# Optimization experiments

Measured on AMD Instinct MI355X. Metric: run time of the kernel, lower is better.

Reference implementation:

```python
import jax
import jax.numpy as jnp
import numpy as np
from jax import lax

GAMMA = 0.99  # cfg.offline_gamma
TAU = 0.95    # cfg.tau (GAE lambda)
T = 4_194_304  # trajectory length (many episodes concatenated, separated by mask=0)


def setup_inputs() -> dict:
    key = jax.random.key(0)
    k1, k2, k3, k4 = jax.random.split(key, 4)
    rewards = jax.random.normal(k1, (T, 1), dtype=jnp.float32)
    values = jax.random.normal(k2, (T, 1), dtype=jnp.float32)        # critic.get_max_value(states)
    next_values = jax.random.normal(k3, (T, 1), dtype=jnp.float32)   # critic.get_max_value(next_states) (bootstrap=True)
    masks = jax.random.randint(k4, (T, 1), 0, 2).astype(jnp.int32)   # 1 = non-terminal, 0 = episode end
    return {"rewards": rewards, "values": values, "next_values": next_values, "masks": masks}


def reference(rewards, values, next_values, masks):
    """Faithful translation of A2C.get_phi's reversed loop as a single lax.scan.

    returns[i]    = r[i] + gamma * (prev_return * m[i] + (1 - m[i]) * next_values[i])
    deltas[i]     = r[i] + gamma * prev_value * m[i] - values[i]
    advantages[i] = deltas[i] + gamma * tau * prev_advantage * m[i]
    with prev_* taken from step i+1 (zeros past the end).
    """
    m = masks.astype(rewards.dtype)  # [T,1]

    def step(carry, xs):
        prev_ret, prev_val, prev_adv = carry  # each [1]
        r, v, nv, mm = xs                     # each [1]
        ret = r + GAMMA * (prev_ret * mm + (1.0 - mm) * nv)
        delta = r + GAMMA * prev_val * mm - v
        adv = delta + GAMMA * TAU * prev_adv * mm
        return (ret, v, adv), (adv, ret)

    zero = jnp.zeros((1,), dtype=rewards.dtype)
    init = (zero, zero, zero)
    _, (advantages, returns) = lax.scan(
        step, init, (rewards, values, next_values, m), reverse=True
    )
    return advantages, returns  # each [T,1]
```

## Files before the change

kernel.cpp:

```cpp
#include <hip/hip_runtime.h>

#define GAMMA 0.99f
#define TAU   0.95f
#define GTAU  (GAMMA * TAU)

constexpr int SEQ   = 16;
constexpr int BLK   = 256;
constexpr int CHUNK = BLK * SEQ;

__device__ __forceinline__ void post_compose(float& A, float& B, float rA, float rB) {
    B = fmaf(A, rB, B);
    A *= rA;
}
__device__ __forceinline__ void pre_compose(float& A, float& B, float lA, float lB) {
    B = fmaf(lA, B, lB);
    A *= lA;
}

__global__ __launch_bounds__(BLK, 4) void k_fused1(
    const float* __restrict__ r, const float* __restrict__ v,
    const float* __restrict__ nv, const int* __restrict__ m,
    float* __restrict__ out_adv, float* __restrict__ out_ret, int T)
{
    const int  tid  = threadIdx.x;
    const int  lane = tid & 63;
    const int  w    = tid >> 6;
    const int  c    = (int)blockIdx.x;
    const long base = (long)c * CHUNK + (long)tid * SEQ;
    const long p    = (long)(c + 1) * CHUNK;

    __shared__ float wSum[4][4];
    __shared__ float s_cb[2];

    float pm = 0.f, pr = 0.f, pv = 0.f, pv1 = 0.f, pnv = 0.f;
    if (w == 0 && p < (long)T) {
        long i = p + lane;
        if (i < (long)T) {
            pm  = (float)m[i];
            pr  = r[i];
            pv  = v[i];
            pv1 = (i + 1 < (long)T) ? v[i + 1] : 0.f;
            pnv = nv[i];
        }
    }

    float delta[SEQ], dd[SEQ];
    unsigned vbits = 0, mbits = 0;
    float Aa = 1.f, Ba = 0.f, Ar = 1.f, Br = 0.f;
    const bool full = (base + SEQ <= (long)T);

    if (full) {
        vbits = 0xFFFFu;
        float rr[SEQ], vv[SEQ + 1], nn[SEQ], fmv[SEQ];
        #pragma unroll
        for (int q = 0; q < SEQ / 4; ++q) {
            float4 t0 = ((const float4*)(r  + base))[q];
            rr[4*q+0]=t0.x; rr[4*q+1]=t0.y; rr[4*q+2]=t0.z; rr[4*q+3]=t0.w;
            float4 t1 = ((const float4*)(v  + base))[q];
            vv[4*q+0]=t1.x; vv[4*q+1]=t1.y; vv[4*q+2]=t1.z; vv[4*q+3]=t1.w;
            float4 t2 = ((const float4*)(nv + base))[q];
            nn[4*q+0]=t2.x; nn[4*q+1]=t2.y; nn[4*q+2]=t2.z; nn[4*q+3]=t2.w;
            int4   t3 = ((const int4*)(m   + base))[q];
            fmv[4*q+0]=(float)t3.x; fmv[4*q+1]=(float)t3.y;
            fmv[4*q+2]=(float)t3.z; fmv[4*q+3]=(float)t3.w;
        }
        vv[SEQ] = (base + SEQ < (long)T) ? v[base + SEQ] : 0.f;
        #pragma unroll
        for (int i = SEQ - 1; i >= 0; --i) {
            if (fmv[i] != 0.f) mbits |= (1u << i);
            delta[i] = rr[i] + GAMMA * fmv[i] * vv[i+1] - vv[i];
            dd[i]    = rr[i] + GAMMA * (1.f - fmv[i]) * nn[i];
            pre_compose(Aa, Ba, GTAU * fmv[i], delta[i]);
            pre_compose(Ar, Br, GAMMA * fmv[i], dd[i]);
        }
    } else {
        #pragma unroll
        for (int ii = 0; ii < SEQ; ++ii) {
            int i = SEQ - 1 - ii;
            long idx = base + i;
            bool val = idx < (long)T;
            float rr  = val ? r[idx]  : 0.f;
            float vv0 = val ? v[idx]  : 0.f;
            float vv1 = (idx + 1 < (long)T) ? v[idx + 1] : 0.f;
            float nn  = val ? nv[idx] : 0.f;
            float fmv = val ? (float)m[idx] : 0.f;
            if (val) vbits |= (1u << i);
            if (val && fmv != 0.f) mbits |= (1u << i);
            delta[i] = val ? (rr + GAMMA * fmv * vv1 - vv0) : 0.f;
            dd[i]    = val ? (rr + GAMMA * (1.f - fmv) * nn) : 0.f;
            pre_compose(Aa, Ba, val ? GTAU * fmv : 1.f, delta[i]);
            pre_compose(Ar, Br, val ? GAMMA * fmv : 1.f, dd[i]);
        }
    }

    #pragma unroll
    for (int st = 1; st < 64; st <<= 1) {
        float oAa = __shfl_down(Aa, st);
        float oBa = __shfl_down(Ba, st);
        float oAr = __shfl_down(Ar, st);
        float oBr = __shfl_down(Br, st);
        if (lane + st < 64) {
            post_compose(Aa, Ba, oAa, oBa);
            post_compose(Ar, Br, oAr, oBr);
        }
    }
    float eAa = __shfl_down(Aa, 1);
    float eBa = __shfl_down(Ba, 1);
    float eAr = __shfl_down(Ar, 1);
    float eBr = __shfl_down(Br, 1);
    if (lane == 63) { eAa=1.f; eBa=0.f; eAr=1.f; eBr=0.f; }

    if (lane == 0) { wSum[w][0]=Aa; wSum[w][1]=Ba; wSum[w][2]=Ar; wSum[w][3]=Br; }
    __syncthreads();

    float WAa=1.f, WBa=0.f, WAr=1.f, WBr=0.f;
    for (int j = 3; j > w; --j) {
        pre_compose(WAa, WBa, wSum[j][0], wSum[j][1]);
        pre_compose(WAr, WBr, wSum[j][2], wSum[j][3]);
    }

    if (w == 0) {
        float MAa=1.f, MBa=0.f, MAr=1.f, MBr=0.f;
        if (p < (long)T) {
            {
                long i = p + lane;
                bool have = i < (long)T;
                float aA=1.f, aB=0.f, rA_=1.f, rB_=0.f;
                if (have) {
                    aA  = GTAU * pm;
                    aB  = pr + GAMMA * pm * pv1 - pv;
                    rA_ = GAMMA * pm;
                    rB_ = pr + GAMMA * (1.f - pm) * pnv;
                }
                bool term = (!have) || (pm == 0.f);
                unsigned long long bz = __ballot(term);
                #pragma unroll
                for (int st = 1; st < 64; st <<= 1) {
                    float oAa = __shfl_down(aA,  st);
                    float oBa = __shfl_down(aB,  st);
                    float oAr = __shfl_down(rA_, st);
                    float oBr = __shfl_down(rB_, st);
                    if (lane + st < 64) {
                        post_compose(aA,  aB,  oAa, oBa);
                        post_compose(rA_, rB_, oAr, oBr);
                    }
                }
                MAa = __shfl(aA, 0);  MBa = __shfl(aB, 0);
                MAr = __shfl(rA_, 0); MBr = __shfl(rB_, 0);
                if (bz != 0ull) goto carry_done;
            }
            for (long jb = p + 64; ; jb += 64) {
                long i = jb + lane;
                bool have = i < (long)T;
                float aA=1.f, aB=0.f, rA_=1.f, rB_=0.f;
                float mi = 0.f;
                if (have) {
                    mi = (float)m[i];
                    float ri  = r[i];
                    float vi  = v[i];
                    float vi1 = (i + 1 < (long)T) ? v[i + 1] : 0.f;
                    float nvi = nv[i];
                    aA  = GTAU * mi;
                    aB  = ri + GAMMA * mi * vi1 - vi;
                    rA_ = GAMMA * mi;
                    rB_ = ri + GAMMA * (1.f - mi) * nvi;
                }
                bool term = (!have) || (mi == 0.f);
                unsigned long long bz = __ballot(term);
                #pragma unroll
                for (int st = 1; st < 64; st <<= 1) {
                    float oAa = __shfl_down(aA,  st);
                    float oBa = __shfl_down(aB,  st);
                    float oAr = __shfl_down(rA_, st);
                    float oBr = __shfl_down(rB_, st);
                    if (lane + st < 64) {
                        post_compose(aA,  aB,  oAa, oBa);
                        post_compose(rA_, rB_, oAr, oBr);
                    }
                }
                float bAa = __shfl(aA, 0),  bBa = __shfl(aB, 0);
                float bAr = __shfl(rA_, 0), bBr = __shfl(rB_, 0);
                post_compose(MAa, MBa, bAa, bBa);
                post_compose(MAr, MBr, bAr, bBr);
                if (bz != 0ull) break;
            }
        }
carry_done:
        if (lane == 0) {
            s_cb[0] = MBa;
            s_cb[1] = MBr;
        }
    }
    __syncthreads();
    const float cbA = s_cb[0];
    const float cbR = s_cb[1];

    float xa = fmaf(WAa, cbA, WBa);
    float xr = fmaf(WAr, cbR, WBr);
    xa = fmaf(eAa, xa, eBa);
    xr = fmaf(eAr, xr, eBr);

    if (full) {
        #pragma unroll
        for (int q = SEQ / 4 - 1; q >= 0; --q) {
            float ta[4], tr[4];
            #pragma unroll
            for (int k = 3; k >= 0; --k) {
                int i = 4 * q + k;
                float a  = (mbits >> i & 1u) ? GTAU  : 0.f;
                float cc = (mbits >> i & 1u) ? GAMMA : 0.f;
                xa = fmaf(a,  xa, delta[i]);
                xr = fmaf(cc, xr, dd[i]);
                ta[k] = xa; tr[k] = xr;
            }
            ((float4*)(out_adv + base))[q] = make_float4(ta[0], ta[1], ta[2], ta[3]);
            ((float4*)(out_ret + base))[q] = make_float4(tr[0], tr[1], tr[2], tr[3]);
        }
    } else {
        #pragma unroll
        for (int i = SEQ - 1; i >= 0; --i) {
            bool val = (vbits >> i) & 1u;
            float a  = val ? ((mbits >> i & 1u) ? GTAU  : 0.f) : 1.f;
            float cc = val ? ((mbits >> i & 1u) ? GAMMA : 0.f) : 1.f;
            xa = fmaf(a,  xa, delta[i]);
            xr = fmaf(cc, xr, dd[i]);
            if (base + i < (long)T) {
                out_adv[base + i] = xa;
                out_ret[base + i] = xr;
            }
        }
    }
}

extern "C" void kernel_launch(void* const* d_in, const int* in_sizes, int n_in,
                              void* d_out, int out_size, void* d_ws, size_t ws_size,
                              hipStream_t stream) {
    const float* r  = (const float*)d_in[0];
    const float* v  = (const float*)d_in[1];
    const float* nv = (const float*)d_in[2];
    const int*   m  = (const int*)d_in[3];
    const int T = in_sizes[0];
    const int nblk = (T + CHUNK - 1) / CHUNK;

    float* out_adv = (float*)d_out;
    float* out_ret = (float*)d_out + T;

    k_fused1<<<nblk, BLK, 0, stream>>>(r, v, nv, m, out_adv, out_ret, T);
}
```

Measured before the change: 26.17 us.

## Shrink per-thread sequence to 4 and share next value via wave shuffle

Reduces elements per thread from 16 to 4, so each thread does a single float4 load per input and the grid has four times as many blocks. The value at the following position is taken from the neighbouring lane with a shuffle rather than reloaded, and full-tile detection moves to wave granularity. The launch-bounds occupancy hint is removed. More blocks means more work in the decoupled carry-propagation chain and more scan overhead per element, traded for lower register pressure and more memory parallelism.

```diff
diff --git a/kernel.cpp b/kernel.cpp
--- a/kernel.cpp
+++ b/kernel.cpp
@@ -4,7 +4,7 @@
 #define TAU   0.95f
 #define GTAU  (GAMMA * TAU)
 
-constexpr int SEQ   = 16;
+constexpr int SEQ   = 4;
 constexpr int BLK   = 256;
 constexpr int CHUNK = BLK * SEQ;
 
@@ -17,7 +17,7 @@
     A *= lA;
 }
 
-__global__ __launch_bounds__(BLK, 4) void k_fused1(
+__global__ __launch_bounds__(BLK) void k_fused1(
     const float* __restrict__ r, const float* __restrict__ v,
     const float* __restrict__ nv, const int* __restrict__ m,
     float* __restrict__ out_adv, float* __restrict__ out_ret, int T)
@@ -47,30 +47,28 @@
     float delta[SEQ], dd[SEQ];
     unsigned vbits = 0, mbits = 0;
     float Aa = 1.f, Ba = 0.f, Ar = 1.f, Br = 0.f;
-    const bool full = (base + SEQ <= (long)T);
-
-    if (full) {
-        vbits = 0xFFFFu;
-        float rr[SEQ], vv[SEQ + 1], nn[SEQ], fmv[SEQ];
-        #pragma unroll
-        for (int q = 0; q < SEQ / 4; ++q) {
-            float4 t0 = ((const float4*)(r  + base))[q];
-            rr[4*q+0]=t0.x; rr[4*q+1]=t0.y; rr[4*q+2]=t0.z; rr[4*q+3]=t0.w;
-            float4 t1 = ((const float4*)(v  + base))[q];
-            vv[4*q+0]=t1.x; vv[4*q+1]=t1.y; vv[4*q+2]=t1.z; vv[4*q+3]=t1.w;
-            float4 t2 = ((const float4*)(nv + base))[q];
-            nn[4*q+0]=t2.x; nn[4*q+1]=t2.y; nn[4*q+2]=t2.z; nn[4*q+3]=t2.w;
-            int4   t3 = ((const int4*)(m   + base))[q];
-            fmv[4*q+0]=(float)t3.x; fmv[4*q+1]=(float)t3.y;
-            fmv[4*q+2]=(float)t3.z; fmv[4*q+3]=(float)t3.w;
-        }
-        vv[SEQ] = (base + SEQ < (long)T) ? v[base + SEQ] : 0.f;
+
+    const bool wfull = ((long)c * CHUNK + (long)(w + 1) * 64 * SEQ) <= (long)T;
+
+    if (wfull) {
+        vbits = 0xFu;
+        float4 r4 = *(const float4*)(r  + base);
+        float4 v4 = *(const float4*)(v  + base);
+        float4 n4 = *(const float4*)(nv + base);
+        int4   m4 = *(const int4*)  (m  + base);
+        float vnext = __shfl_down(v4.x, 1);
+        if (lane == 63) vnext = (base + SEQ < (long)T) ? v[base + SEQ] : 0.f;
+
+        float rr[4]  = {r4.x, r4.y, r4.z, r4.w};
+        float vv[5]  = {v4.x, v4.y, v4.z, v4.w, vnext};
+        float nn[4]  = {n4.x, n4.y, n4.z, n4.w};
+        float fmv[4] = {(float)m4.x, (float)m4.y, (float)m4.z, (float)m4.w};
         #pragma unroll
         for (int i = SEQ - 1; i >= 0; --i) {
             if (fmv[i] != 0.f) mbits |= (1u << i);
             delta[i] = rr[i] + GAMMA * fmv[i] * vv[i+1] - vv[i];
             dd[i]    = rr[i] + GAMMA * (1.f - fmv[i]) * nn[i];
-            pre_compose(Aa, Ba, GTAU * fmv[i], delta[i]);
+            pre_compose(Aa, Ba, GTAU  * fmv[i], delta[i]);
             pre_compose(Ar, Br, GAMMA * fmv[i], dd[i]);
         }
     } else {
@@ -88,7 +86,7 @@
             if (val && fmv != 0.f) mbits |= (1u << i);
             delta[i] = val ? (rr + GAMMA * fmv * vv1 - vv0) : 0.f;
             dd[i]    = val ? (rr + GAMMA * (1.f - fmv) * nn) : 0.f;
-            pre_compose(Aa, Ba, val ? GTAU * fmv : 1.f, delta[i]);
+            pre_compose(Aa, Ba, val ? GTAU * fmv  : 1.f, delta[i]);
             pre_compose(Ar, Br, val ? GAMMA * fmv : 1.f, dd[i]);
         }
     }
@@ -200,22 +198,18 @@
     xa = fmaf(eAa, xa, eBa);
     xr = fmaf(eAr, xr, eBr);
 
-    if (full) {
-        #pragma unroll
-        for (int q = SEQ / 4 - 1; q >= 0; --q) {
-            float ta[4], tr[4];
-            #pragma unroll
-            for (int k = 3; k >= 0; --k) {
-                int i = 4 * q + k;
-                float a  = (mbits >> i & 1u) ? GTAU  : 0.f;
-                float cc = (mbits >> i & 1u) ? GAMMA : 0.f;
-                xa = fmaf(a,  xa, delta[i]);
-                xr = fmaf(cc, xr, dd[i]);
-                ta[k] = xa; tr[k] = xr;
-            }
-            ((float4*)(out_adv + base))[q] = make_float4(ta[0], ta[1], ta[2], ta[3]);
-            ((float4*)(out_ret + base))[q] = make_float4(tr[0], tr[1], tr[2], tr[3]);
-        }
+    if (wfull) {
+        float ta[4], tr[4];
+        #pragma unroll
+        for (int i = SEQ - 1; i >= 0; --i) {
+            float a  = (mbits >> i & 1u) ? GTAU  : 0.f;
+            float cc = (mbits >> i & 1u) ? GAMMA : 0.f;
+            xa = fmaf(a,  xa, delta[i]);
+            xr = fmaf(cc, xr, dd[i]);
+            ta[i] = xa; tr[i] = xr;
+        }
+        *(float4*)(out_adv + base) = make_float4(ta[0], ta[1], ta[2], ta[3]);
+        *(float4*)(out_ret + base) = make_float4(tr[0], tr[1], tr[2], tr[3]);
     } else {
         #pragma unroll
         for (int i = SEQ - 1; i >= 0; --i) {
```

New measurement: 24.23 us. 1.08x faster.
